# Kernel optimization log

Measured on AMD Instinct MI355X. Metric: run time of the kernel, lower is better.

Reference implementation:

```python
import jax, jax.numpy as jnp
import numpy as np

B = 524288      # batch
D = 16          # ds_dim
N = 32          # number of dynamical systems
H = 128         # gating hidden width


def setup_inputs() -> dict:
    key = jax.random.key(0)
    ks = jax.random.split(key, 8)
    x_cur = jax.random.normal(ks[0], (B, D), dtype=jnp.float32)
    W1 = jax.random.normal(ks[1], (H, D), dtype=jnp.float32) * 0.1
    b1 = jax.random.normal(ks[2], (H,), dtype=jnp.float32) * 0.1
    W2 = jax.random.normal(ks[3], (N, H), dtype=jnp.float32) * 0.1
    b2 = jax.random.normal(ks[4], (N,), dtype=jnp.float32) * 0.1
    # B matrices are PSD (geotorch.positive_semidefinite), C are skew-symmetric (geotorch.skew)
    Braw = jax.random.normal(ks[5], (N, D, D), dtype=jnp.float32) * 0.3
    B_mats = jnp.einsum('nij,nkj->nik', Braw, Braw)  # PSD: R R^T
    Craw = jax.random.normal(ks[6], (N, D, D), dtype=jnp.float32) * 0.3
    C_mats = 0.5 * (Craw - jnp.swapaxes(Craw, -1, -2))  # skew-symmetric
    x_target = jax.random.normal(ks[7], (1, D), dtype=jnp.float32)
    return {"x_cur": x_cur, "W1": W1, "b1": b1, "W2": W2, "b2": b2,
            "B_mats": B_mats, "C_mats": C_mats, "x_target": x_target}


def reference(x_cur, W1, b1, W2, b2, B_mats, C_mats, x_target):
    # gating weights: softmax(Linear -> ReLU -> Linear)
    h = jax.nn.relu(x_cur @ W1.T + b1)          # [B, H]
    w_all = jax.nn.softmax(h @ W2.T + b2, axis=1)  # [B, N]
    # per-system linear map A_i = B_i + C_i applied to (x* - x)
    A = B_mats + C_mats                          # [N, D, D]
    diff = x_target - x_cur                      # [B, D]
    # torch.mm(A, diff.T).T == diff @ A.T -> proj[b,n,k] = sum_d A[n,k,d] diff[b,d]
    proj = jnp.einsum('nkd,bd->bnk', A, diff)    # [B, N, D]
    out = jnp.einsum('bn,bnk->bk', w_all, proj)  # [B, D]
    return out
```

## Files before the change

kernel.cpp:

```cpp
#include <hip/hip_runtime.h>

#define BATCH 524288

typedef __bf16 bf16x8 __attribute__((ext_vector_type(8)));
typedef __bf16 bf16x2 __attribute__((ext_vector_type(2)));
typedef float f32x4 __attribute__((ext_vector_type(4)));
typedef float f32x8 __attribute__((ext_vector_type(8)));
typedef float f32x2 __attribute__((ext_vector_type(2)));
typedef int   i32x4 __attribute__((ext_vector_type(4)));

#define SW1 16384
#define SZC 20480
#define SW2 20512
#define SB2 28704
#define SXT 28832
#define SB1 28896
#define SHC 30944
#define NWAVES 8
#define SMEM_BYTES (30944 + NWAVES * 2560)

__device__ __forceinline__ f32x8 load8(const float* __restrict__ p) {
    float4 a = *(const float4*)p;
    float4 b = *(const float4*)(p + 4);
    f32x8 v = {a.x, a.y, a.z, a.w, b.x, b.y, b.z, b.w};
    return v;
}

__device__ __forceinline__ int pack2bf(float a, float b) {
    f32x2 v = {a, b};
    bf16x2 p = __builtin_convertvector(v, bf16x2);
    return __builtin_bit_cast(int, p);
}

__global__ __launch_bounds__(512, 3) void andp_v15(
    const float* __restrict__ x_cur,
    const float* __restrict__ W1,
    const float* __restrict__ b1,
    const float* __restrict__ W2,
    const float* __restrict__ b2,
    const float* __restrict__ Bm,
    const float* __restrict__ Cm,
    const float* __restrict__ x_t,
    float* __restrict__ out)
{
    extern __shared__ char smem[];
    int* sA2i = (int*)smem;
    int* sW1i = (int*)(smem + SW1);
    int* sW2i = (int*)(smem + SW2);
    const int tid = threadIdx.x;

#pragma unroll
    for (int i = 0; i < 8; ++i) {
        int o2 = tid + i * 512;
        int o  = o2 * 2;
        int kk = o >> 9, qp = (o >> 7) & 3, k = (o >> 3) & 15, j = o & 7;
        int n = 2 * kk + (qp >> 1), d = (qp & 1) * 8 + j;
        int src = n * 256 + k * 16 + d;
        float2 bv = *(const float2*)(Bm + src);
        float2 cv = *(const float2*)(Cm + src);
        sA2i[o2] = pack2bf(bv.x + cv.x, bv.y + cv.y);
    }
#pragma unroll
    for (int i = 0; i < 2; ++i) {
        int o2 = tid + i * 512;
        int o  = o2 * 2;
        int t = o >> 8, qq = (o >> 7) & 1, cc = (o >> 3) & 15, j = o & 7;
        int src = (t * 16 + cc) * 16 + qq * 8 + j;
        float2 v = *(const float2*)(W1 + src);
        sW1i[o2] = pack2bf(v.x, v.y);
    }
    if (tid < 8) ((int*)(smem + SZC))[tid] = 0;
#pragma unroll
    for (int i = 0; i < 4; ++i) {
        int o2 = tid + i * 512;
        int chunk = o2 >> 8, rem = o2 & 255;
        int ln = rem >> 2, j2 = rem & 3;
        int qq = ln >> 4, cc = ln & 15;
        int t2 = chunk >> 2, s = chunk & 3;
        int src = (t2 * 16 + cc) * 128 + s * 32 + 4 * qq + j2;
        sW2i[o2] = pack2bf(W2[src], W2[src + 16]);
    }
    if (tid < 32) ((float*)(smem + SB2))[tid] = b2[tid];
    if (tid < 16) ((float*)(smem + SXT))[tid] = x_t[tid];
    if (tid < 128) {
        float v = b1[tid];
        ((float4*)(smem + SB1))[tid] = make_float4(v, v, v, v);
    }

    const int wave = tid >> 6, lane = tid & 63;
    const int c = lane & 15, q = lane >> 4;
    const int qh = q >> 1;
    const int hh = (q & 1) * 8;
    const int c4 = c * 4;

    const char* sW1f = smem + SW1;
    const int w1base = (q < 2) ? ((q * 16 + c) * 16) : (SZC - SW1);
    const int w1step = (q < 2) ? 512 : 0;
    const char* sW2f = smem + SW2 + lane * 16;
    __bf16* hcw0 = (__bf16*)(smem + SHC + wave * 2560);
    __bf16* hcw1 = hcw0 + 640;
    const float* sB2f = (const float*)(smem + SB2);
    const float* sXTf = (const float*)(smem + SXT);
    const float* sB1r = (const float*)(smem + SB1);

    __syncthreads();

    const int blk_row = blockIdx.x * 512 + wave * 64;
    const f32x4 z4 = {0.f, 0.f, 0.f, 0.f};

    const f32x4 bq0 = *(const f32x4*)(sB2f + q * 4);
    const f32x4 bq1 = *(const f32x4*)(sB2f + 16 + q * 4);

    bf16x8 af[2];
#pragma unroll
    for (int t01 = 0; t01 < 2; ++t01) {
        f32x8 xv = load8(x_cur + (size_t)(blk_row + t01 * 16 + c) * 16 + hh);
        af[t01] = __builtin_convertvector(xv, bf16x8);
    }

#pragma unroll 1
    for (int p = 0; p < 2; ++p) {
        const int r0 = blk_row + p * 32;

        f32x4 acc2[2][2];
        acc2[0][0] = bq0; acc2[0][1] = bq1; acc2[1][0] = bq0; acc2[1][1] = bq1;
#pragma unroll
        for (int s = 0; s < 4; ++s) {
            f32x4 cba = *(const f32x4*)(sB1r + ((2 * s) * 16 + c) * 4);
            f32x4 cbb = *(const f32x4*)(sB1r + ((2 * s + 1) * 16 + c) * 4);
#pragma unroll
            for (int t01 = 0; t01 < 2; ++t01) {
                __bf16* hcw = t01 ? hcw1 : hcw0;
                bf16x8 w1a = *(const bf16x8*)(sW1f + w1base + (2 * s) * w1step);
                bf16x8 w1b = *(const bf16x8*)(sW1f + w1base + (2 * s + 1) * w1step);
                f32x4 a1a = __builtin_amdgcn_mfma_f32_16x16x32_bf16(af[t01], w1a, cba, 0, 0, 0);
                f32x4 a1b = __builtin_amdgcn_mfma_f32_16x16x32_bf16(af[t01], w1b, cbb, 0, 0, 0);
#pragma unroll
                for (int r = 0; r < 4; ++r) {
                    float va = fmaxf(a1a[r], 0.f);
                    float vb = fmaxf(a1b[r], 0.f);
                    *(int*)(hcw + (q * 4 + r) * 40 + 2 * c) = pack2bf(va, vb);
                }
            }
#pragma unroll
            for (int t01 = 0; t01 < 2; ++t01) {
                __bf16* hcw = t01 ? hcw1 : hcw0;
                bf16x8 hb = *(const bf16x8*)(hcw + c * 40 + q * 8);
                bf16x8 w20 = *(const bf16x8*)(sW2f + (0 * 4 + s) * 1024);
                bf16x8 w21 = *(const bf16x8*)(sW2f + (1 * 4 + s) * 1024);
                acc2[t01][0] = __builtin_amdgcn_mfma_f32_16x16x32_bf16(w20, hb, acc2[t01][0], 0, 0, 0);
                acc2[t01][1] = __builtin_amdgcn_mfma_f32_16x16x32_bf16(w21, hb, acc2[t01][1], 0, 0, 0);
            }
        }

        bf16x8 afn0 = af[0], afn1 = af[1];
        if (p == 0) {
            f32x8 xv0 = load8(x_cur + (size_t)(blk_row + 32 + c) * 16 + hh);
            f32x8 xv1 = load8(x_cur + (size_t)(blk_row + 48 + c) * 16 + hh);
            afn0 = __builtin_convertvector(xv0, bf16x8);
            afn1 = __builtin_convertvector(xv1, bf16x8);
        }

        int wq[8];
        {
            float e0[8], e1[8], sum0 = 0.f, sum1 = 0.f;
#pragma unroll
            for (int r = 0; r < 4; ++r) {
                e0[r]     = __expf(acc2[0][0][r]);
                e0[4 + r] = __expf(acc2[0][1][r]);
                e1[r]     = __expf(acc2[1][0][r]);
                e1[4 + r] = __expf(acc2[1][1][r]);
                sum0 += e0[r] + e0[4 + r];
                sum1 += e1[r] + e1[4 + r];
            }
            sum0 += __shfl_xor(sum0, 16, 64);
            sum0 += __shfl_xor(sum0, 32, 64);
            sum1 += __shfl_xor(sum1, 16, 64);
            sum1 += __shfl_xor(sum1, 32, 64);
            float inv0 = 1.0f / sum0;
            float inv1 = 1.0f / sum1;
#pragma unroll
            for (int i = 0; i < 8; ++i)
                wq[i] = pack2bf(e0[i] * inv0, e1[i] * inv1);
        }

        f32x8 dif[2];
        {
            f32x4 xta = *(const f32x4*)(sXTf + hh);
            f32x4 xtb = *(const f32x4*)(sXTf + hh + 4);
            f32x8 xtv = {xta[0], xta[1], xta[2], xta[3], xtb[0], xtb[1], xtb[2], xtb[3]};
            dif[0] = xtv - __builtin_convertvector(af[0], f32x8);
            dif[1] = xtv - __builtin_convertvector(af[1], f32x8);
        }

        int sel[16];
#pragma unroll
        for (int kk = 0; kk < 16; ++kk) {
            const int lo = (kk >> 3) * 4 + 2 * (kk & 1);
            const int bpi = c4 + ((kk >> 1) & 3) * 64;
            int bpA = __builtin_amdgcn_ds_bpermute(bpi, wq[lo]);
            int bpB = __builtin_amdgcn_ds_bpermute(bpi, wq[lo + 1]);
            sel[kk] = qh ? bpB : bpA;
        }

        f32x4 acc3[2];
        acc3[0] = z4; acc3[1] = z4;
#pragma unroll
        for (int kk = 0; kk < 16; ++kk) {
            float w0 = __builtin_bit_cast(float, (unsigned)sel[kk] << 16);
            float w1 = __builtin_bit_cast(float, (unsigned)sel[kk] & 0xffff0000u);
            f32x2 w0p = {w0, w0}, w1p = {w1, w1};
            i32x4 g0i, g1i;
#pragma unroll
            for (int jj = 0; jj < 4; ++jj) {
                f32x2 d0 = {dif[0][2 * jj], dif[0][2 * jj + 1]};
                f32x2 d1 = {dif[1][2 * jj], dif[1][2 * jj + 1]};
                f32x2 p0 = d0 * w0p;
                f32x2 p1 = d1 * w1p;
                g0i[jj] = pack2bf(p0[0], p0[1]);
                g1i[jj] = pack2bf(p1[0], p1[1]);
            }
            bf16x8 a2f = *(const bf16x8*)(smem + kk * 1024 + lane * 16);
            bf16x8 g0 = __builtin_bit_cast(bf16x8, g0i);
            bf16x8 g1 = __builtin_bit_cast(bf16x8, g1i);
            acc3[0] = __builtin_amdgcn_mfma_f32_16x16x32_bf16(a2f, g0, acc3[0], 0, 0, 0);
            acc3[1] = __builtin_amdgcn_mfma_f32_16x16x32_bf16(a2f, g1, acc3[1], 0, 0, 0);
        }

#pragma unroll
        for (int t01 = 0; t01 < 2; ++t01) {
            float4 st = make_float4(acc3[t01][0], acc3[t01][1], acc3[t01][2], acc3[t01][3]);
            *(float4*)(out + (size_t)(r0 + t01 * 16 + c) * 16 + q * 4) = st;
        }

        af[0] = afn0;
        af[1] = afn1;
    }
}

extern "C" void kernel_launch(void* const* d_in, const int* in_sizes, int n_in,
                              void* d_out, int out_size, void* d_ws, size_t ws_size,
                              hipStream_t stream) {
    const float* x_cur = (const float*)d_in[0];
    const float* W1    = (const float*)d_in[1];
    const float* b1    = (const float*)d_in[2];
    const float* W2    = (const float*)d_in[3];
    const float* b2    = (const float*)d_in[4];
    const float* Bm    = (const float*)d_in[5];
    const float* Cm    = (const float*)d_in[6];
    const float* x_t   = (const float*)d_in[7];
    float* out = (float*)d_out;

    const int blocks = BATCH / 512;
    andp_v15<<<blocks, 512, SMEM_BYTES, stream>>>(
        x_cur, W1, b1, W2, b2, Bm, Cm, x_t, out);
}
```

Measured before the change: 119.7 us.

## Hoist W1/W2 fragments and biases into registers, lower occupancy bound

Loads the W1 and W2 bf16 MFMA fragments, the b1 biases, x_target and b2 into registers once per wave instead of re-reading them from LDS every iteration. The b1 bias is now added after the MFMA instead of being used as the accumulator init, so the replicated float4 b1 copy in shared memory goes away and the LDS footprint shrinks. The bpermute selection loop is merged into the MFMA loop. Launch bounds drop from 3 to 2 blocks per CU to make room for the extra registers, which risks lower occupancy and less latency hiding.

```diff
diff --git a/kernel.cpp b/kernel.cpp
--- a/kernel.cpp
+++ b/kernel.cpp
@@ -15,9 +15,9 @@
 #define SB2 28704
 #define SXT 28832
 #define SB1 28896
-#define SHC 30944
+#define SHC 29408
 #define NWAVES 8
-#define SMEM_BYTES (30944 + NWAVES * 2560)
+#define SMEM_BYTES (29408 + NWAVES * 2560)
 
 __device__ __forceinline__ f32x8 load8(const float* __restrict__ p) {
     float4 a = *(const float4*)p;
@@ -32,7 +32,7 @@
     return __builtin_bit_cast(int, p);
 }
 
-__global__ __launch_bounds__(512, 3) void andp_v15(
+__global__ __launch_bounds__(512, 2) void andp_v16(
     const float* __restrict__ x_cur,
     const float* __restrict__ W1,
     const float* __restrict__ b1,
@@ -82,10 +82,7 @@
     }
     if (tid < 32) ((float*)(smem + SB2))[tid] = b2[tid];
     if (tid < 16) ((float*)(smem + SXT))[tid] = x_t[tid];
-    if (tid < 128) {
-        float v = b1[tid];
-        ((float4*)(smem + SB1))[tid] = make_float4(v, v, v, v);
-    }
+    if (tid < 128) ((float*)(smem + SB1))[tid] = b1[tid];
 
     const int wave = tid >> 6, lane = tid & 63;
     const int c = lane & 15, q = lane >> 4;
@@ -101,15 +98,30 @@
     __bf16* hcw1 = hcw0 + 640;
     const float* sB2f = (const float*)(smem + SB2);
     const float* sXTf = (const float*)(smem + SXT);
-    const float* sB1r = (const float*)(smem + SB1);
+    const float* sB1f = (const float*)(smem + SB1);
 
     __syncthreads();
+
+    bf16x8 w1f[8], w2f[8];
+#pragma unroll
+    for (int i = 0; i < 8; ++i) {
+        w1f[i] = *(const bf16x8*)(sW1f + w1base + i * w1step);
+        w2f[i] = *(const bf16x8*)(sW2f + i * 1024);
+    }
+    float b1v[8];
+#pragma unroll
+    for (int t = 0; t < 8; ++t) b1v[t] = sB1f[t * 16 + c];
+    f32x8 xtv;
+    {
+        f32x4 xta = *(const f32x4*)(sXTf + hh);
+        f32x4 xtb = *(const f32x4*)(sXTf + hh + 4);
+        xtv = (f32x8){xta[0], xta[1], xta[2], xta[3], xtb[0], xtb[1], xtb[2], xtb[3]};
+    }
+    const f32x4 bq0 = *(const f32x4*)(sB2f + q * 4);
+    const f32x4 bq1 = *(const f32x4*)(sB2f + 16 + q * 4);
 
     const int blk_row = blockIdx.x * 512 + wave * 64;
     const f32x4 z4 = {0.f, 0.f, 0.f, 0.f};
-
-    const f32x4 bq0 = *(const f32x4*)(sB2f + q * 4);
-    const f32x4 bq1 = *(const f32x4*)(sB2f + 16 + q * 4);
 
     bf16x8 af[2];
 #pragma unroll
@@ -126,19 +138,17 @@
         acc2[0][0] = bq0; acc2[0][1] = bq1; acc2[1][0] = bq0; acc2[1][1] = bq1;
 #pragma unroll
         for (int s = 0; s < 4; ++s) {
-            f32x4 cba = *(const f32x4*)(sB1r + ((2 * s) * 16 + c) * 4);
-            f32x4 cbb = *(const f32x4*)(sB1r + ((2 * s + 1) * 16 + c) * 4);
+            float b1a = b1v[2 * s];
+            float b1b = b1v[2 * s + 1];
 #pragma unroll
             for (int t01 = 0; t01 < 2; ++t01) {
                 __bf16* hcw = t01 ? hcw1 : hcw0;
-                bf16x8 w1a = *(const bf16x8*)(sW1f + w1base + (2 * s) * w1step);
-                bf16x8 w1b = *(const bf16x8*)(sW1f + w1base + (2 * s + 1) * w1step);
-                f32x4 a1a = __builtin_amdgcn_mfma_f32_16x16x32_bf16(af[t01], w1a, cba, 0, 0, 0);
-                f32x4 a1b = __builtin_amdgcn_mfma_f32_16x16x32_bf16(af[t01], w1b, cbb, 0, 0, 0);
+                f32x4 a1a = __builtin_amdgcn_mfma_f32_16x16x32_bf16(af[t01], w1f[2 * s], z4, 0, 0, 0);
+                f32x4 a1b = __builtin_amdgcn_mfma_f32_16x16x32_bf16(af[t01], w1f[2 * s + 1], z4, 0, 0, 0);
 #pragma unroll
                 for (int r = 0; r < 4; ++r) {
-                    float va = fmaxf(a1a[r], 0.f);
-                    float vb = fmaxf(a1b[r], 0.f);
+                    float va = fmaxf(a1a[r] + b1a, 0.f);
+                    float vb = fmaxf(a1b[r] + b1b, 0.f);
                     *(int*)(hcw + (q * 4 + r) * 40 + 2 * c) = pack2bf(va, vb);
                 }
             }
@@ -146,10 +156,8 @@
             for (int t01 = 0; t01 < 2; ++t01) {
                 __bf16* hcw = t01 ? hcw1 : hcw0;
                 bf16x8 hb = *(const bf16x8*)(hcw + c * 40 + q * 8);
-                bf16x8 w20 = *(const bf16x8*)(sW2f + (0 * 4 + s) * 1024);
-                bf16x8 w21 = *(const bf16x8*)(sW2f + (1 * 4 + s) * 1024);
-                acc2[t01][0] = __builtin_amdgcn_mfma_f32_16x16x32_bf16(w20, hb, acc2[t01][0], 0, 0, 0);
-                acc2[t01][1] = __builtin_amdgcn_mfma_f32_16x16x32_bf16(w21, hb, acc2[t01][1], 0, 0, 0);
+                acc2[t01][0] = __builtin_amdgcn_mfma_f32_16x16x32_bf16(w2f[s], hb, acc2[t01][0], 0, 0, 0);
+                acc2[t01][1] = __builtin_amdgcn_mfma_f32_16x16x32_bf16(w2f[4 + s], hb, acc2[t01][1], 0, 0, 0);
             }
         }
 
@@ -185,30 +193,20 @@
         }
 
         f32x8 dif[2];
-        {
-            f32x4 xta = *(const f32x4*)(sXTf + hh);
-            f32x4 xtb = *(const f32x4*)(sXTf + hh + 4);
-            f32x8 xtv = {xta[0], xta[1], xta[2], xta[3], xtb[0], xtb[1], xtb[2], xtb[3]};
-            dif[0] = xtv - __builtin_convertvector(af[0], f32x8);
-            dif[1] = xtv - __builtin_convertvector(af[1], f32x8);
-        }
-
-        int sel[16];
+        dif[0] = xtv - __builtin_convertvector(af[0], f32x8);
+        dif[1] = xtv - __builtin_convertvector(af[1], f32x8);
+
+        f32x4 acc3[2];
+        acc3[0] = z4; acc3[1] = z4;
 #pragma unroll
         for (int kk = 0; kk < 16; ++kk) {
             const int lo = (kk >> 3) * 4 + 2 * (kk & 1);
             const int bpi = c4 + ((kk >> 1) & 3) * 64;
             int bpA = __builtin_amdgcn_ds_bpermute(bpi, wq[lo]);
             int bpB = __builtin_amdgcn_ds_bpermute(bpi, wq[lo + 1]);
-            sel[kk] = qh ? bpB : bpA;
-        }
-
-        f32x4 acc3[2];
-        acc3[0] = z4; acc3[1] = z4;
-#pragma unroll
-        for (int kk = 0; kk < 16; ++kk) {
-            float w0 = __builtin_bit_cast(float, (unsigned)sel[kk] << 16);
-            float w1 = __builtin_bit_cast(float, (unsigned)sel[kk] & 0xffff0000u);
+            int sel = qh ? bpB : bpA;
+            float w0 = __builtin_bit_cast(float, (unsigned)sel << 16);
+            float w1 = __builtin_bit_cast(float, (unsigned)sel & 0xffff0000u);
             f32x2 w0p = {w0, w0}, w1p = {w1, w1};
             i32x4 g0i, g1i;
 #pragma unroll
@@ -252,6 +250,6 @@
     float* out = (float*)d_out;
 
     const int blocks = BATCH / 512;
-    andp_v15<<<blocks, 512, SMEM_BYTES, stream>>>(
+    andp_v16<<<blocks, 512, SMEM_BYTES, stream>>>(
         x_cur, W1, b1, W2, b2, Bm, Cm, x_t, out);
 }
```

Result: slower. 122.7 us (+2.5%).

## Apply gating weights after MFMA instead of scaling diff before each MFMA

Applied to the files above, without the earlier changes.

Rather than forming weighted, bf16-packed diff vectors per system before every MFMA, the kernel converts diff to bf16 once. It splits diff into even and odd K-half operands by zeroing the other half, runs unweighted MFMAs, and scales the fp32 results by the gating weights. This removes the per-iteration multiply and pack VALU work. In exchange it doubles the MFMA count (four per kk instead of two), half of which multiply zeros, and adds fp32 FMAs on the accumulators.

```diff
diff --git a/kernel.cpp b/kernel.cpp
--- a/kernel.cpp
+++ b/kernel.cpp
@@ -7,7 +7,6 @@
 typedef float f32x4 __attribute__((ext_vector_type(4)));
 typedef float f32x8 __attribute__((ext_vector_type(8)));
 typedef float f32x2 __attribute__((ext_vector_type(2)));
-typedef int   i32x4 __attribute__((ext_vector_type(4)));
 
 #define SW1 16384
 #define SZC 20480
@@ -32,7 +31,7 @@
     return __builtin_bit_cast(int, p);
 }
 
-__global__ __launch_bounds__(512, 3) void andp_v15(
+__global__ __launch_bounds__(512, 3) void andp_v18(
     const float* __restrict__ x_cur,
     const float* __restrict__ W1,
     const float* __restrict__ b1,
@@ -89,7 +88,6 @@
 
     const int wave = tid >> 6, lane = tid & 63;
     const int c = lane & 15, q = lane >> 4;
-    const int qh = q >> 1;
     const int hh = (q & 1) * 8;
     const int c4 = c * 4;
 
@@ -184,47 +182,40 @@
                 wq[i] = pack2bf(e0[i] * inv0, e1[i] * inv1);
         }
 
-        f32x8 dif[2];
+        bf16x8 difbE[2], difbO[2];
         {
             f32x4 xta = *(const f32x4*)(sXTf + hh);
             f32x4 xtb = *(const f32x4*)(sXTf + hh + 4);
             f32x8 xtv = {xta[0], xta[1], xta[2], xta[3], xtb[0], xtb[1], xtb[2], xtb[3]};
-            dif[0] = xtv - __builtin_convertvector(af[0], f32x8);
-            dif[1] = xtv - __builtin_convertvector(af[1], f32x8);
-        }
-
-        int sel[16];
+            bf16x8 d0 = __builtin_convertvector(xtv - __builtin_convertvector(af[0], f32x8), bf16x8);
+            bf16x8 d1 = __builtin_convertvector(xtv - __builtin_convertvector(af[1], f32x8), bf16x8);
+            const bf16x8 zb = {};
+            bool lowK = (q < 2);
+            difbE[0] = lowK ? d0 : zb;
+            difbE[1] = lowK ? d1 : zb;
+            difbO[0] = lowK ? zb : d0;
+            difbO[1] = lowK ? zb : d1;
+        }
+
+        f32x4 acc3[2];
+        acc3[0] = z4; acc3[1] = z4;
 #pragma unroll
         for (int kk = 0; kk < 16; ++kk) {
             const int lo = (kk >> 3) * 4 + 2 * (kk & 1);
             const int bpi = c4 + ((kk >> 1) & 3) * 64;
             int bpA = __builtin_amdgcn_ds_bpermute(bpi, wq[lo]);
             int bpB = __builtin_amdgcn_ds_bpermute(bpi, wq[lo + 1]);
-            sel[kk] = qh ? bpB : bpA;
-        }
-
-        f32x4 acc3[2];
-        acc3[0] = z4; acc3[1] = z4;
-#pragma unroll
-        for (int kk = 0; kk < 16; ++kk) {
-            float w0 = __builtin_bit_cast(float, (unsigned)sel[kk] << 16);
-            float w1 = __builtin_bit_cast(float, (unsigned)sel[kk] & 0xffff0000u);
-            f32x2 w0p = {w0, w0}, w1p = {w1, w1};
-            i32x4 g0i, g1i;
-#pragma unroll
-            for (int jj = 0; jj < 4; ++jj) {
-                f32x2 d0 = {dif[0][2 * jj], dif[0][2 * jj + 1]};
-                f32x2 d1 = {dif[1][2 * jj], dif[1][2 * jj + 1]};
-                f32x2 p0 = d0 * w0p;
-                f32x2 p1 = d1 * w1p;
-                g0i[jj] = pack2bf(p0[0], p0[1]);
-                g1i[jj] = pack2bf(p1[0], p1[1]);
-            }
             bf16x8 a2f = *(const bf16x8*)(smem + kk * 1024 + lane * 16);
-            bf16x8 g0 = __builtin_bit_cast(bf16x8, g0i);
-            bf16x8 g1 = __builtin_bit_cast(bf16x8, g1i);
-            acc3[0] = __builtin_amdgcn_mfma_f32_16x16x32_bf16(a2f, g0, acc3[0], 0, 0, 0);
-            acc3[1] = __builtin_amdgcn_mfma_f32_16x16x32_bf16(a2f, g1, acc3[1], 0, 0, 0);
+            f32x4 prE0 = __builtin_amdgcn_mfma_f32_16x16x32_bf16(a2f, difbE[0], z4, 0, 0, 0);
+            f32x4 prO0 = __builtin_amdgcn_mfma_f32_16x16x32_bf16(a2f, difbO[0], z4, 0, 0, 0);
+            f32x4 prE1 = __builtin_amdgcn_mfma_f32_16x16x32_bf16(a2f, difbE[1], z4, 0, 0, 0);
+            f32x4 prO1 = __builtin_amdgcn_mfma_f32_16x16x32_bf16(a2f, difbO[1], z4, 0, 0, 0);
+            float wA0 = __builtin_bit_cast(float, (unsigned)bpA << 16);
+            float wA1 = __builtin_bit_cast(float, (unsigned)bpA & 0xffff0000u);
+            float wB0 = __builtin_bit_cast(float, (unsigned)bpB << 16);
+            float wB1 = __builtin_bit_cast(float, (unsigned)bpB & 0xffff0000u);
+            acc3[0] += wA0 * prE0 + wB0 * prO0;
+            acc3[1] += wA1 * prE1 + wB1 * prO1;
         }
 
 #pragma unroll
@@ -252,6 +243,6 @@
     float* out = (float*)d_out;
 
     const int blocks = BATCH / 512;
-    andp_v15<<<blocks, 512, SMEM_BYTES, stream>>>(
+    andp_v18<<<blocks, 512, SMEM_BYTES, stream>>>(
         x_cur, W1, b1, W2, b2, Bm, Cm, x_t, out);
 }
```

After: 119.3 us. No clear change (-0.3%).
